# Performance work log

Measured on AMD Instinct MI355X. Metric: run time of the kernel, lower is better.

Reference implementation:

```python
import jax, jax.numpy as jnp
import numpy as np


def setup_inputs() -> dict:
    key = jax.random.key(0)
    ks = jax.random.split(key, 6)
    B, N, D, E = 16, 64, 256, 256
    nodes = jax.random.normal(ks[0], (B * N, D), jnp.float32)
    edges = jax.random.normal(ks[1], (B * N * N, E), jnp.float32)
    W_in = jax.random.normal(ks[2], (2 * D + E, D), jnp.float32) / np.float32(np.sqrt(2 * D + E))
    b_in = jnp.zeros((D,), jnp.float32)
    W_coef = jax.random.normal(ks[3], (D, 1), jnp.float32) / np.float32(np.sqrt(D))
    b_coef = jnp.zeros((1,), jnp.float32)
    W_out = jax.random.normal(ks[4], (D, D), jnp.float32) / np.float32(np.sqrt(D))
    b_out = jnp.zeros((D,), jnp.float32)
    return {"nodes": nodes, "edges": edges, "W_in": W_in, "b_in": b_in,
            "W_coef": W_coef, "b_coef": b_coef, "W_out": W_out, "b_out": b_out,
            "B": B, "N": N}


def reference(nodes, edges, W_in, b_in, W_coef, b_coef, W_out, b_out, B, N):
    # Uniform nums = [N]*B special case of the ragged torch loop.
    D = nodes.shape[-1]
    n3 = nodes.reshape(B, N, D)
    # pair[b,i,j] = [node_i, node_j, edge_ij]  -> [B,N,N,2D+E]
    pair = jnp.concatenate([
        jnp.broadcast_to(n3[:, :, None, :], (B, N, N, D)),
        jnp.broadcast_to(n3[:, None, :, :], (B, N, N, D)),
        edges.reshape(B, N, N, -1),
    ], axis=-1)
    h = jax.nn.relu(pair @ W_in + b_in)            # [B,N,N,D]
    coefs = h @ W_coef + b_coef                    # [B,N,N,1]
    diag = jnp.eye(N, dtype=coefs.dtype)[None, :, :, None] * jnp.float32(1e9)
    attn = jax.nn.softmax(coefs - diag, axis=2)    # softmax over j, diag masked
    residual = jnp.sum(attn * h, axis=2)           # [B,N,D]
    new_nodes = nodes + jax.nn.relu(residual.reshape(B * N, D) @ W_out + b_out)
    return new_nodes, h.reshape(B * N * N, D)
```

## Files before the change

### kernel.cpp

```cpp
#include <hip/hip_runtime.h>
#include <hip/hip_bf16.h>

typedef unsigned int u32;
typedef unsigned short u16;
typedef __attribute__((ext_vector_type(8))) short bf16x8;
typedef __attribute__((ext_vector_type(4))) float f32x4;

#define DI __device__ __forceinline__

DI u16 f2bfu(float f){
  union{float f; u32 i;} u; u.f = f;
  u32 lsb = (u.i >> 16) & 1u;
  u.i += 0x7fffu + lsb;
  return (u16)(u.i >> 16);
}

union BU { uint4 v; bf16x8 s; };

__global__ __launch_bounds__(256) void k_pack(const float* __restrict__ W_in,
                                              u16* __restrict__ Wp3,
                                              u16* __restrict__ Wp12)
{
  int idx = blockIdx.x * 256 + threadIdx.x;
  int l = idx & 63;
  int g = idx >> 6;
  int lq = l >> 4, lr = l & 15;
  u16 o[8];
  if (g < 128){
    int nt = g >> 3, kk = g & 7;
    int n  = nt * 16 + lr;
    int k0 = 512 + kk * 32 + lq * 8;
#pragma unroll
    for (int tt = 0; tt < 8; tt++) o[tt] = f2bfu(W_in[(size_t)(k0 + tt) * 256 + n]);
    *(uint4*)(Wp3 + (size_t)idx * 8) = *(uint4*)o;
  } else {
    int g2 = g - 128;
    int half = g2 >> 7, rem = g2 & 127;
    int nt = rem >> 3, kk = rem & 7;
    int n  = nt * 16 + lr;
    int k0 = half * 256 + kk * 32 + lq * 8;
#pragma unroll
    for (int tt = 0; tt < 8; tt++) o[tt] = f2bfu(W_in[(size_t)(k0 + tt) * 256 + n]);
    *(uint4*)(Wp12 + (size_t)g2 * 512 + (size_t)l * 8) = *(uint4*)o;
  }
}

__global__ __launch_bounds__(256) void k_pre(
    const float* __restrict__ nodes, const float* __restrict__ b_in,
    const u16* __restrict__ Wp12, float* __restrict__ P1, float* __restrict__ P2)
{
  const int t = threadIdx.x;
  const int w = t >> 6, l = t & 63, lq = l >> 4, lr = l & 15;
  const int rt = blockIdx.x >> 1, half = blockIdx.x & 1;

  bf16x8 af[8];
  {
    const float* ap = nodes + (size_t)(rt * 64 + 16 * w + lr) * 256 + lq * 8;
#pragma unroll
    for (int kk = 0; kk < 8; kk++){
      float4 x = *(const float4*)(ap + kk * 32);
      float4 y = *(const float4*)(ap + kk * 32 + 4);
      bf16x8 a;
      a[0]=(short)f2bfu(x.x); a[1]=(short)f2bfu(x.y); a[2]=(short)f2bfu(x.z); a[3]=(short)f2bfu(x.w);
      a[4]=(short)f2bfu(y.x); a[5]=(short)f2bfu(y.y); a[6]=(short)f2bfu(y.z); a[7]=(short)f2bfu(y.w);
      af[kk] = a;
    }
  }
  const uint4* wp = (const uint4*)(Wp12 + (size_t)half * 128 * 512);
  float* P = half ? P2 : P1;
#pragma unroll
  for (int nt = 0; nt < 16; nt++){
    f32x4 acc = {0.f, 0.f, 0.f, 0.f};
#pragma unroll
    for (int kk = 0; kk < 8; kk++){
      BU bu; bu.v = wp[(nt * 8 + kk) * 64 + l];
      acc = __builtin_amdgcn_mfma_f32_16x16x32_bf16(af[kk], bu.s, acc, 0, 0, 0);
    }
    const int col = nt * 16 + lr;
    const float bv = half ? 0.f : b_in[col];
#pragma unroll
    for (int r = 0; r < 4; r++){
      const int row = rt * 64 + 16 * w + 4 * lq + r;
      P[(size_t)row * 256 + col] = acc[r] + bv;
    }
  }
}

__global__ __launch_bounds__(256) void k_main(
    const float* __restrict__ nodes, const float* __restrict__ edges,
    const u16* __restrict__ Wp3, const float* __restrict__ W_coef,
    const float* __restrict__ b_coef, const float* __restrict__ W_out,
    const float* __restrict__ b_out, const float* __restrict__ P1,
    const float* __restrict__ P2, float* __restrict__ out_nodes,
    float* __restrict__ out_h)
{
  __shared__ float hS[64 * 256];
  __shared__ float coefS[64];
  __shared__ float attnS[64];
  __shared__ float resS[256];

  const int t = threadIdx.x;
  const int w = t >> 6, l = t & 63, lq = l >> 4, lr = l & 15;
  const int bi = blockIdx.x;
  const int b = bi >> 6, i = bi & 63;

  bf16x8 af[8];
  {
    const float* ap = edges + (size_t)bi * 16384 + (size_t)(16 * w + lr) * 256 + lq * 8;
#pragma unroll
    for (int kk = 0; kk < 8; kk++){
      float4 x = *(const float4*)(ap + kk * 32);
      float4 y = *(const float4*)(ap + kk * 32 + 4);
      bf16x8 a;
      a[0]=(short)f2bfu(x.x); a[1]=(short)f2bfu(x.y); a[2]=(short)f2bfu(x.z); a[3]=(short)f2bfu(x.w);
      a[4]=(short)f2bfu(y.x); a[5]=(short)f2bfu(y.y); a[6]=(short)f2bfu(y.z); a[7]=(short)f2bfu(y.w);
      af[kk] = a;
    }
  }

  const uint4* wp = (const uint4*)Wp3;
  float cpart[4] = {0.f, 0.f, 0.f, 0.f};
#pragma unroll
  for (int nt = 0; nt < 16; nt++){
    f32x4 acc = {0.f, 0.f, 0.f, 0.f};
#pragma unroll
    for (int kk = 0; kk < 8; kk++){
      BU bu; bu.v = wp[(nt * 8 + kk) * 64 + l];
      acc = __builtin_amdgcn_mfma_f32_16x16x32_bf16(af[kk], bu.s, acc, 0, 0, 0);
    }
    const int col = nt * 16 + lr;
    const float p1 = P1[(size_t)bi * 256 + col];
    const float wc = W_coef[col];
#pragma unroll
    for (int r = 0; r < 4; r++){
      const int row = 16 * w + 4 * lq + r;
      const float p2 = P2[((size_t)b * 64 + row) * 256 + col];
      float h = acc[r] + p1 + p2;
      h = h > 0.f ? h : 0.f;
      hS[row * 256 + col] = h;
      out_h[((size_t)bi * 64 + row) * 256 + col] = h;
      cpart[r] += h * wc;
    }
  }

#pragma unroll
  for (int r = 0; r < 4; r++){
    float v = cpart[r];
    v += __shfl_xor(v, 1, 64);
    v += __shfl_xor(v, 2, 64);
    v += __shfl_xor(v, 4, 64);
    v += __shfl_xor(v, 8, 64);
    if (lr == 0) coefS[16 * w + 4 * lq + r] = v;
  }
  __syncthreads();

  if (t < 64){
    int j = t;
    float val = coefS[j] + b_coef[0] - (j == i ? 1e9f : 0.f);
    float m = val;
#pragma unroll
    for (int off = 32; off >= 1; off >>= 1){ float o = __shfl_xor(m, off, 64); m = m > o ? m : o; }
    float e = __expf(val - m);
    float s = e;
#pragma unroll
    for (int off = 32; off >= 1; off >>= 1) s += __shfl_xor(s, off, 64);
    attnS[j] = e / s;
  }
  __syncthreads();

  {
    const int d = t;
    float res = 0.f;
#pragma unroll 8
    for (int j = 0; j < 64; j++) res += attnS[j] * hS[j * 256 + d];
    resS[d] = res;
  }
  __syncthreads();

  {
    const int d = t;
    float acco = b_out[d];
    for (int k4 = 0; k4 < 64; k4++){
      float4 r4 = *(const float4*)&resS[k4 * 4];
      acco += r4.x * W_out[(size_t)(k4 * 4 + 0) * 256 + d];
      acco += r4.y * W_out[(size_t)(k4 * 4 + 1) * 256 + d];
      acco += r4.z * W_out[(size_t)(k4 * 4 + 2) * 256 + d];
      acco += r4.w * W_out[(size_t)(k4 * 4 + 3) * 256 + d];
    }
    float nv = nodes[(size_t)bi * 256 + d];
    out_nodes[(size_t)bi * 256 + d] = nv + (acco > 0.f ? acco : 0.f);
  }
}

extern "C" void kernel_launch(void* const* d_in, const int* in_sizes, int n_in,
                              void* d_out, int out_size, void* d_ws, size_t ws_size,
                              hipStream_t stream)
{
  const float* nodes  = (const float*)d_in[0];
  const float* edges  = (const float*)d_in[1];
  const float* W_in   = (const float*)d_in[2];
  const float* b_in   = (const float*)d_in[3];
  const float* W_coef = (const float*)d_in[4];
  const float* b_coef = (const float*)d_in[5];
  const float* W_out  = (const float*)d_in[6];
  const float* b_out  = (const float*)d_in[7];
  (void)in_sizes; (void)n_in; (void)out_size; (void)ws_size;

  float* P1  = (float*)d_ws;
  float* P2  = P1 + 262144;
  u16*  Wp3  = (u16*)(P2 + 262144);
  u16*  Wp12 = Wp3 + 65536;

  float* out_nodes = (float*)d_out;
  float* out_h = out_nodes + 262144;

  hipLaunchKernelGGL(k_pack, dim3(96),   dim3(256), 0, stream, W_in, Wp3, Wp12);
  hipLaunchKernelGGL(k_pre,  dim3(32),   dim3(256), 0, stream, nodes, b_in, Wp12, P1, P2);
  hipLaunchKernelGGL(k_main, dim3(1024), dim3(256), 0, stream,
                     nodes, edges, Wp3, W_coef, b_coef, W_out, b_out,
                     P1, P2, out_nodes, out_h);
}
```

Baseline: 183.5 us.

## Keep h in registers, stage weights via async LDS loads, widen k_pre grid

k_main drops the 64KB shared h tile and keeps the post-ReLU h values in MFMA accumulator registers. The attention-weighted sum is computed from those registers with cross-lane shuffles and a small per-wave reduction buffer. The packed edge weights are double-buffered into LDS through global_load_lds, and launch bounds request 3 blocks per CU to raise occupancy. k_pre is split over 4x more blocks, each handling a quarter of the output tiles. The risks are higher register pressure from 16 accumulator vectors and extra barriers in the weight pipeline.

```diff
diff --git a/kernel.cpp b/kernel.cpp
--- a/kernel.cpp
+++ b/kernel.cpp
@@ -16,6 +16,12 @@
 }
 
 union BU { uint4 v; bf16x8 s; };
+
+DI void gld16(const void* g, void* l){
+  __builtin_amdgcn_global_load_lds(
+      (const __attribute__((address_space(1))) void*)g,
+      (__attribute__((address_space(3))) void*)l, 16, 0, 0);
+}
 
 __global__ __launch_bounds__(256) void k_pack(const float* __restrict__ W_in,
                                               u16* __restrict__ Wp3,
@@ -51,7 +57,8 @@
 {
   const int t = threadIdx.x;
   const int w = t >> 6, l = t & 63, lq = l >> 4, lr = l & 15;
-  const int rt = blockIdx.x >> 1, half = blockIdx.x & 1;
+  const int bid = blockIdx.x;
+  const int rt = bid >> 3, half = (bid >> 2) & 1, cg = bid & 3;
 
   bf16x8 af[8];
   {
@@ -69,7 +76,8 @@
   const uint4* wp = (const uint4*)(Wp12 + (size_t)half * 128 * 512);
   float* P = half ? P2 : P1;
 #pragma unroll
-  for (int nt = 0; nt < 16; nt++){
+  for (int ntl = 0; ntl < 4; ntl++){
+    const int nt = cg * 4 + ntl;
     f32x4 acc = {0.f, 0.f, 0.f, 0.f};
 #pragma unroll
     for (int kk = 0; kk < 8; kk++){
@@ -86,7 +94,7 @@
   }
 }
 
-__global__ __launch_bounds__(256) void k_main(
+__global__ __launch_bounds__(256, 3) void k_main(
     const float* __restrict__ nodes, const float* __restrict__ edges,
     const u16* __restrict__ Wp3, const float* __restrict__ W_coef,
     const float* __restrict__ b_coef, const float* __restrict__ W_out,
@@ -94,15 +102,27 @@
     const float* __restrict__ P2, float* __restrict__ out_nodes,
     float* __restrict__ out_h)
 {
-  __shared__ float hS[64 * 256];
+  __shared__ uint4 wS[2][1024];
   __shared__ float coefS[64];
   __shared__ float attnS[64];
+  __shared__ float resW[4][256];
   __shared__ float resS[256];
 
   const int t = threadIdx.x;
   const int w = t >> 6, l = t & 63, lq = l >> 4, lr = l & 15;
   const int bi = blockIdx.x;
   const int b = bi >> 6, i = bi & 63;
+
+  const char* wp3b = (const char*)Wp3;
+  auto stage = [&](int bufi, int ntc){
+    const char* src = wp3b + (size_t)ntc * 16384;
+    char* dst = (char*)&wS[bufi][0];
+#pragma unroll
+    for (int c = 0; c < 4; ++c)
+      gld16(src + c * 4096 + w * 1024 + l * 16, dst + c * 4096 + w * 1024);
+  };
+
+  stage(0, 0);
 
   bf16x8 af[8];
   {
@@ -118,29 +138,44 @@
     }
   }
 
-  const uint4* wp = (const uint4*)Wp3;
+  const float* p1p = P1 + (size_t)bi * 256;
+  const float* p2p = P2 + (size_t)b * 64 * 256;
+
+  f32x4 acc[16];
+#pragma unroll
+  for (int nt = 0; nt < 16; nt++) acc[nt] = (f32x4){0.f, 0.f, 0.f, 0.f};
   float cpart[4] = {0.f, 0.f, 0.f, 0.f};
-#pragma unroll
-  for (int nt = 0; nt < 16; nt++){
-    f32x4 acc = {0.f, 0.f, 0.f, 0.f};
-#pragma unroll
-    for (int kk = 0; kk < 8; kk++){
-      BU bu; bu.v = wp[(nt * 8 + kk) * 64 + l];
-      acc = __builtin_amdgcn_mfma_f32_16x16x32_bf16(af[kk], bu.s, acc, 0, 0, 0);
-    }
-    const int col = nt * 16 + lr;
-    const float p1 = P1[(size_t)bi * 256 + col];
-    const float wc = W_coef[col];
-#pragma unroll
-    for (int r = 0; r < 4; r++){
-      const int row = 16 * w + 4 * lq + r;
-      const float p2 = P2[((size_t)b * 64 + row) * 256 + col];
-      float h = acc[r] + p1 + p2;
-      h = h > 0.f ? h : 0.f;
-      hS[row * 256 + col] = h;
-      out_h[((size_t)bi * 64 + row) * 256 + col] = h;
-      cpart[r] += h * wc;
-    }
+
+  __syncthreads();
+  int buf = 0;
+#pragma unroll
+  for (int ntc = 0; ntc < 8; ntc++){
+    if (ntc < 7) stage(buf ^ 1, ntc + 1);
+#pragma unroll
+    for (int nt2 = 0; nt2 < 2; nt2++){
+      const int nt = ntc * 2 + nt2;
+      const u16* wsb = (const u16*)&wS[buf][nt2 * 512];
+#pragma unroll
+      for (int kk = 0; kk < 8; kk++){
+        BU bu; bu.v = *(const uint4*)(wsb + (size_t)(kk * 64 + l) * 8);
+        acc[nt] = __builtin_amdgcn_mfma_f32_16x16x32_bf16(af[kk], bu.s, acc[nt], 0, 0, 0);
+      }
+      const int col = nt * 16 + lr;
+      const float p1 = p1p[col];
+      const float wc = W_coef[col];
+#pragma unroll
+      for (int r = 0; r < 4; r++){
+        const int row = 16 * w + 4 * lq + r;
+        const float p2 = p2p[row * 256 + col];
+        float h = acc[nt][r] + p1 + p2;
+        h = h > 0.f ? h : 0.f;
+        acc[nt][r] = h;
+        out_h[((size_t)bi * 64 + row) * 256 + col] = h;
+        cpart[r] += h * wc;
+      }
+    }
+    __syncthreads();
+    buf ^= 1;
   }
 
 #pragma unroll
@@ -169,17 +204,26 @@
   __syncthreads();
 
   {
-    const int d = t;
-    float res = 0.f;
-#pragma unroll 8
-    for (int j = 0; j < 64; j++) res += attnS[j] * hS[j * 256 + d];
-    resS[d] = res;
-  }
+    const float a0 = attnS[16 * w + 4 * lq + 0];
+    const float a1 = attnS[16 * w + 4 * lq + 1];
+    const float a2 = attnS[16 * w + 4 * lq + 2];
+    const float a3 = attnS[16 * w + 4 * lq + 3];
+#pragma unroll
+    for (int nt = 0; nt < 16; nt++){
+      float part = a0 * acc[nt][0] + a1 * acc[nt][1] + a2 * acc[nt][2] + a3 * acc[nt][3];
+      part += __shfl_xor(part, 16, 64);
+      part += __shfl_xor(part, 32, 64);
+      if (lq == (nt & 3)) resW[w][nt * 16 + lr] = part;
+    }
+  }
+  __syncthreads();
+  resS[t] = resW[0][t] + resW[1][t] + resW[2][t] + resW[3][t];
   __syncthreads();
 
   {
     const int d = t;
     float acco = b_out[d];
+#pragma unroll 8
     for (int k4 = 0; k4 < 64; k4++){
       float4 r4 = *(const float4*)&resS[k4 * 4];
       acco += r4.x * W_out[(size_t)(k4 * 4 + 0) * 256 + d];
@@ -215,7 +259,7 @@
   float* out_h = out_nodes + 262144;
 
   hipLaunchKernelGGL(k_pack, dim3(96),   dim3(256), 0, stream, W_in, Wp3, Wp12);
-  hipLaunchKernelGGL(k_pre,  dim3(32),   dim3(256), 0, stream, nodes, b_in, Wp12, P1, P2);
+  hipLaunchKernelGGL(k_pre,  dim3(128),  dim3(256), 0, stream, nodes, b_in, Wp12, P1, P2);
   hipLaunchKernelGGL(k_main, dim3(1024), dim3(256), 0, stream,
                      nodes, edges, Wp3, W_coef, b_coef, W_out, b_out,
                      P1, P2, out_nodes, out_h);
```

Measured after the change: 172.4 us. 1.06x faster.

## Drop 64KB LDS tile, transpose MFMA operands, split pre-GEMM across more blocks

Applied to the files above, without the earlier changes.

k_main no longer stages the 64x256 h tile in shared memory. It re-reads h from global out_h (likely L2-resident) for the attention sum, so several blocks can fit per CU (launch bounds 4). The MFMA operands are swapped so each lane holds four consecutive d values, which allows float4 stores and loads of P1/P2/W_coef and a simpler coef reduction. The Wp3 pack order is changed to match. Edge loads are batched before conversion, blocks are swizzled across batches, and k_pre is split four ways over column groups to launch 128 blocks. The risk is extra global traffic from re-reading h, and a possible read-after-write visibility issue within the block through global memory.

```diff
diff --git a/kernel.cpp b/kernel.cpp
--- a/kernel.cpp
+++ b/kernel.cpp
@@ -5,6 +5,7 @@
 typedef unsigned short u16;
 typedef __attribute__((ext_vector_type(8))) short bf16x8;
 typedef __attribute__((ext_vector_type(4))) float f32x4;
+typedef __attribute__((ext_vector_type(4))) float f4;
 
 #define DI __device__ __forceinline__
 
@@ -27,7 +28,7 @@
   int lq = l >> 4, lr = l & 15;
   u16 o[8];
   if (g < 128){
-    int nt = g >> 3, kk = g & 7;
+    int kk = g >> 4, nt = g & 15;
     int n  = nt * 16 + lr;
     int k0 = 512 + kk * 32 + lq * 8;
 #pragma unroll
@@ -51,7 +52,8 @@
 {
   const int t = threadIdx.x;
   const int w = t >> 6, l = t & 63, lq = l >> 4, lr = l & 15;
-  const int rt = blockIdx.x >> 1, half = blockIdx.x & 1;
+  const int bid = blockIdx.x;
+  const int rt = bid >> 3, half = (bid >> 2) & 1, cg = bid & 3;
 
   bf16x8 af[8];
   {
@@ -69,7 +71,8 @@
   const uint4* wp = (const uint4*)(Wp12 + (size_t)half * 128 * 512);
   float* P = half ? P2 : P1;
 #pragma unroll
-  for (int nt = 0; nt < 16; nt++){
+  for (int ntl = 0; ntl < 4; ntl++){
+    const int nt = cg * 4 + ntl;
     f32x4 acc = {0.f, 0.f, 0.f, 0.f};
 #pragma unroll
     for (int kk = 0; kk < 8; kk++){
@@ -86,7 +89,7 @@
   }
 }
 
-__global__ __launch_bounds__(256) void k_main(
+__global__ __launch_bounds__(256, 4) void k_main(
     const float* __restrict__ nodes, const float* __restrict__ edges,
     const u16* __restrict__ Wp3, const float* __restrict__ W_coef,
     const float* __restrict__ b_coef, const float* __restrict__ W_out,
@@ -94,69 +97,80 @@
     const float* __restrict__ P2, float* __restrict__ out_nodes,
     float* __restrict__ out_h)
 {
-  __shared__ float hS[64 * 256];
   __shared__ float coefS[64];
   __shared__ float attnS[64];
   __shared__ float resS[256];
 
   const int t = threadIdx.x;
   const int w = t >> 6, l = t & 63, lq = l >> 4, lr = l & 15;
-  const int bi = blockIdx.x;
+  const int bid = blockIdx.x;
+  const int bi = ((bid & 7) << 7) | (bid >> 3);
   const int b = bi >> 6, i = bi & 63;
+  const int j = 16 * w + lr;
 
   bf16x8 af[8];
   {
-    const float* ap = edges + (size_t)bi * 16384 + (size_t)(16 * w + lr) * 256 + lq * 8;
-#pragma unroll
-    for (int kk = 0; kk < 8; kk++){
-      float4 x = *(const float4*)(ap + kk * 32);
-      float4 y = *(const float4*)(ap + kk * 32 + 4);
+    const float* ap = edges + (size_t)bi * 16384 + (size_t)j * 256 + lq * 8;
+    float4 x[8], y[8];
+#pragma unroll
+    for (int kk = 0; kk < 8; kk++){
+      x[kk] = *(const float4*)(ap + kk * 32);
+      y[kk] = *(const float4*)(ap + kk * 32 + 4);
+    }
+#pragma unroll
+    for (int kk = 0; kk < 8; kk++){
       bf16x8 a;
-      a[0]=(short)f2bfu(x.x); a[1]=(short)f2bfu(x.y); a[2]=(short)f2bfu(x.z); a[3]=(short)f2bfu(x.w);
-      a[4]=(short)f2bfu(y.x); a[5]=(short)f2bfu(y.y); a[6]=(short)f2bfu(y.z); a[7]=(short)f2bfu(y.w);
+      a[0]=(short)f2bfu(x[kk].x); a[1]=(short)f2bfu(x[kk].y); a[2]=(short)f2bfu(x[kk].z); a[3]=(short)f2bfu(x[kk].w);
+      a[4]=(short)f2bfu(y[kk].x); a[5]=(short)f2bfu(y[kk].y); a[6]=(short)f2bfu(y[kk].z); a[7]=(short)f2bfu(y[kk].w);
       af[kk] = a;
     }
   }
 
   const uint4* wp = (const uint4*)Wp3;
-  float cpart[4] = {0.f, 0.f, 0.f, 0.f};
-#pragma unroll
-  for (int nt = 0; nt < 16; nt++){
-    f32x4 acc = {0.f, 0.f, 0.f, 0.f};
-#pragma unroll
-    for (int kk = 0; kk < 8; kk++){
-      BU bu; bu.v = wp[(nt * 8 + kk) * 64 + l];
-      acc = __builtin_amdgcn_mfma_f32_16x16x32_bf16(af[kk], bu.s, acc, 0, 0, 0);
-    }
-    const int col = nt * 16 + lr;
-    const float p1 = P1[(size_t)bi * 256 + col];
-    const float wc = W_coef[col];
-#pragma unroll
-    for (int r = 0; r < 4; r++){
-      const int row = 16 * w + 4 * lq + r;
-      const float p2 = P2[((size_t)b * 64 + row) * 256 + col];
-      float h = acc[r] + p1 + p2;
-      h = h > 0.f ? h : 0.f;
-      hS[row * 256 + col] = h;
-      out_h[((size_t)bi * 64 + row) * 256 + col] = h;
-      cpart[r] += h * wc;
-    }
-  }
-
-#pragma unroll
-  for (int r = 0; r < 4; r++){
-    float v = cpart[r];
-    v += __shfl_xor(v, 1, 64);
-    v += __shfl_xor(v, 2, 64);
-    v += __shfl_xor(v, 4, 64);
-    v += __shfl_xor(v, 8, 64);
-    if (lr == 0) coefS[16 * w + 4 * lq + r] = v;
-  }
+  const float* p1p = P1 + (size_t)bi * 256;
+  const float* p2p = P2 + ((size_t)b * 64 + j) * 256;
+  float* hop = out_h + ((size_t)bi * 64 + j) * 256;
+  float cpart = 0.f;
+
+  for (int half = 0; half < 2; ++half){
+    f32x4 acc[8];
+#pragma unroll
+    for (int n8 = 0; n8 < 8; n8++) acc[n8] = (f32x4){0.f, 0.f, 0.f, 0.f};
+    const uint4* wph = wp + (size_t)half * 8 * 64;
+#pragma unroll
+    for (int n8 = 0; n8 < 8; n8++){
+#pragma unroll
+      for (int kk = 0; kk < 8; kk++){
+        BU bu; bu.v = wph[(size_t)(kk * 16 + n8) * 64 + l];
+        acc[n8] = __builtin_amdgcn_mfma_f32_16x16x32_bf16(bu.s, af[kk], acc[n8], 0, 0, 0);
+      }
+    }
+    const int dbase = half * 128;
+#pragma unroll
+    for (int n8 = 0; n8 < 8; n8++){
+      const int d0 = dbase + n8 * 16 + 4 * lq;
+      f4 p1v = *(const f4*)(p1p + d0);
+      f4 p2v = *(const f4*)(p2p + d0);
+      f4 wcv = *(const f4*)(W_coef + d0);
+      f4 h;
+#pragma unroll
+      for (int r = 0; r < 4; r++){
+        float xx = acc[n8][r] + p1v[r] + p2v[r];
+        h[r] = xx > 0.f ? xx : 0.f;
+      }
+      *(f4*)(hop + d0) = h;
+      cpart += h[0]*wcv[0] + h[1]*wcv[1] + h[2]*wcv[2] + h[3]*wcv[3];
+    }
+  }
+
+  cpart += __shfl_xor(cpart, 16, 64);
+  cpart += __shfl_xor(cpart, 32, 64);
+  if (lq == 0) coefS[j] = cpart;
   __syncthreads();
 
   if (t < 64){
-    int j = t;
-    float val = coefS[j] + b_coef[0] - (j == i ? 1e9f : 0.f);
+    int jj = t;
+    float val = coefS[jj] + b_coef[0] - (jj == i ? 1e9f : 0.f);
     float m = val;
 #pragma unroll
     for (int off = 32; off >= 1; off >>= 1){ float o = __shfl_xor(m, off, 64); m = m > o ? m : o; }
@@ -164,22 +178,23 @@
     float s = e;
 #pragma unroll
     for (int off = 32; off >= 1; off >>= 1) s += __shfl_xor(s, off, 64);
-    attnS[j] = e / s;
+    attnS[jj] = e / s;
   }
   __syncthreads();
 
   {
-    const int d = t;
+    const float* hb = out_h + (size_t)bi * 16384;
     float res = 0.f;
 #pragma unroll 8
-    for (int j = 0; j < 64; j++) res += attnS[j] * hS[j * 256 + d];
-    resS[d] = res;
+    for (int jj = 0; jj < 64; jj++) res += attnS[jj] * hb[(size_t)jj * 256 + t];
+    resS[t] = res;
   }
   __syncthreads();
 
   {
     const int d = t;
     float acco = b_out[d];
+#pragma unroll 8
     for (int k4 = 0; k4 < 64; k4++){
       float4 r4 = *(const float4*)&resS[k4 * 4];
       acco += r4.x * W_out[(size_t)(k4 * 4 + 0) * 256 + d];
@@ -215,7 +230,7 @@
   float* out_h = out_nodes + 262144;
 
   hipLaunchKernelGGL(k_pack, dim3(96),   dim3(256), 0, stream, W_in, Wp3, Wp12);
-  hipLaunchKernelGGL(k_pre,  dim3(32),   dim3(256), 0, stream, nodes, b_in, Wp12, P1, P2);
+  hipLaunchKernelGGL(k_pre,  dim3(128),  dim3(256), 0, stream, nodes, b_in, Wp12, P1, P2);
   hipLaunchKernelGGL(k_main, dim3(1024), dim3(256), 0, stream,
                      nodes, edges, Wp3, W_coef, b_coef, W_out, b_out,
                      P1, P2, out_nodes, out_h);
```

Measured after the change: 190.4 us. 1.04x slower.
